# Optimization experiments

Measured on AMD Instinct MI355X. Metric: run time of the kernel, lower is better.

The kernel has to match this reference:

```python
import jax, jax.numpy as jnp
import numpy as np
from jax import lax

B, C, H, W, K = 32, 128, 56, 56, 5
CR = C // 4          # reduced channels in weight-gen MLP
CE = 4 * C           # expanded channels
EPS = 1e-6


def setup_inputs() -> dict:
    key = jax.random.key(0)
    ks = jax.random.split(key, 8)
    s = lambda fan: 1.0 / np.sqrt(fan)
    return {
        "x": jax.random.normal(ks[0], (B, C, H, W), jnp.float32),
        "w_fc1": jax.random.normal(ks[1], (CR, C), jnp.float32) * s(C),
        "ln1_w": jnp.ones((CR,), jnp.float32),
        "ln1_b": jnp.zeros((CR,), jnp.float32),
        "w_fc2": jax.random.normal(ks[2], (C * K * K, CR), jnp.float32) * s(CR),
        "ln2_w": jnp.ones((C,), jnp.float32),
        "ln2_b": jnp.zeros((C,), jnp.float32),
        "w_expand": jax.random.normal(ks[3], (CE, C), jnp.float32) * s(C),
        "w_shrink": jax.random.normal(ks[4], (C, CE), jnp.float32) * s(CE),
        "grn_gamma": jax.random.normal(ks[5], (CE,), jnp.float32) * 0.1,
        "grn_beta": jax.random.normal(ks[6], (CE,), jnp.float32) * 0.1,
    }


def _ln(v, w, b, axis):
    u = v.mean(axis, keepdims=True)
    s2 = jnp.square(v - u).mean(axis, keepdims=True)
    return (v - u) * lax.rsqrt(s2 + EPS) * w + b


def reference(x, w_fc1, ln1_w, ln1_b, w_fc2, ln2_w, ln2_b, w_expand, w_shrink,
              grn_gamma, grn_beta):
    b, c, h, w = x.shape
    # ---- dynamic weight generation: pool -> fc1 -> LN -> fc2 ----
    pooled = x.mean((2, 3))                                  # [B, C]
    hdn = pooled @ w_fc1.T                                   # [B, CR]
    hdn = _ln(hdn, ln1_w, ln1_b, axis=-1)                    # channels_first LN over CR
    dyn = hdn @ w_fc2.T                                      # [B, C*K*K]
    dyn_w = dyn.reshape(b * c, 1, K, K)                      # per-sample depthwise kernels
    # ---- per-sample dynamic depthwise conv (groups = B*C) ----
    pad = K // 2
    out = lax.conv_general_dilated(
        x.reshape(1, b * c, h, w), dyn_w,
        window_strides=(1, 1), padding=[(pad, pad), (pad, pad)],
        dimension_numbers=("NCHW", "OIHW", "NCHW"),
        feature_group_count=b * c,
    ).reshape(b, c, h, w)
    # ---- LN (channels_first) over channel dim ----
    u = out.mean(1, keepdims=True)
    s2 = jnp.square(out - u).mean(1, keepdims=True)
    out = (out - u) * lax.rsqrt(s2 + EPS)
    out = ln2_w[None, :, None, None] * out + ln2_b[None, :, None, None]
    # ---- expand 1x1 -> GELU -> GRN -> shrink 1x1 ----
    out = jnp.einsum("bchw,oc->bohw", out, w_expand)         # [B, 4C, H, W]
    out = jax.nn.gelu(out, approximate=False)
    gx = jnp.sqrt(jnp.sum(jnp.square(out), axis=(2, 3), keepdims=True))  # [B,4C,1,1]
    nx = gx / (gx.mean(1, keepdims=True) + EPS)
    g = grn_gamma[None, :, None, None]
    bt = grn_beta[None, :, None, None]
    out = g * (out * nx) + bt + out
    out = jnp.einsum("bohw,co->bchw", out, w_shrink)         # [B, C, H, W]
    return out + x
```

## Files before the change

### kernel.cpp

```cpp
#include <hip/hip_runtime.h>
#include <hip/hip_bf16.h>

#define B_   32
#define C_   128
#define H_   56
#define W_   56
#define HW_  (H_*W_)
#define BHW_ (B_*HW_)
#define K5_  5
#define KK_  25
#define CR_  32
#define CE_  512
#define EPS_ 1e-6f

typedef __hip_bfloat16 bf16;
typedef __attribute__((ext_vector_type(8))) short short8;
typedef __attribute__((ext_vector_type(4))) float f32x4;


__device__ __forceinline__ float wave_reduce_sum(float v) {
#pragma unroll
  for (int off = 32; off > 0; off >>= 1) v += __shfl_down(v, off, 64);
  return v;
}
__device__ __forceinline__ float bf2f(unsigned short u) {
  return __uint_as_float(((unsigned)u) << 16);
}
__device__ __forceinline__ unsigned short f2bf_bits(float f) {
  bf16 h = __float2bfloat16(f);
  unsigned short u;
  __builtin_memcpy(&u, &h, 2);
  return u;
}
__device__ __forceinline__ float fast_gelu(float v) {
  float t = __expf(-1.702f * v);
  return v * __builtin_amdgcn_rcpf(1.0f + t);
}

__global__ __launch_bounds__(256) void prep_kernel(const float* __restrict__ we,
                                                   bf16* __restrict__ weB) {
  int i = blockIdx.x * 256 + threadIdx.x;
  if (i < CE_ * C_) weB[i] = __float2bfloat16(we[i]);
}

__global__ __launch_bounds__(256) void pool_kernel(const float* __restrict__ x,
                                                   float* __restrict__ pooled) {
  int bc = blockIdx.x;
  const float* xp = x + (size_t)bc * HW_;
  float s = 0.f;
  for (int i = threadIdx.x; i < HW_; i += 256) s += xp[i];
  s = wave_reduce_sum(s);
  __shared__ float red[4];
  int lane = threadIdx.x & 63, wid = threadIdx.x >> 6;
  if (lane == 0) red[wid] = s;
  __syncthreads();
  if (threadIdx.x == 0) pooled[bc] = (red[0] + red[1] + red[2] + red[3]) * (1.0f / HW_);
}

__global__ __launch_bounds__(256) void fc_kernel(const float* __restrict__ pooled,
                                                 const float* __restrict__ w_fc1,
                                                 const float* __restrict__ ln1_w,
                                                 const float* __restrict__ ln1_b,
                                                 const float* __restrict__ w_fc2,
                                                 float* __restrict__ dyn) {
  int b = blockIdx.x;
  int tid = threadIdx.x;
  __shared__ float sp[C_];
  __shared__ float sh[CR_];
  __shared__ float shn[CR_];
  __shared__ float stats[2];
  if (tid < C_) sp[tid] = pooled[b * C_ + tid];
  __syncthreads();
  if (tid < CR_) {
    float acc = 0.f;
    const float* wr = w_fc1 + tid * C_;
#pragma unroll 4
    for (int c = 0; c < C_; ++c) acc += sp[c] * wr[c];
    sh[tid] = acc;
  }
  __syncthreads();
  if (tid == 0) {
    float u = 0.f;
    for (int j = 0; j < CR_; ++j) u += sh[j];
    u *= (1.0f / CR_);
    float v = 0.f;
    for (int j = 0; j < CR_; ++j) { float d = sh[j] - u; v += d * d; }
    v *= (1.0f / CR_);
    stats[0] = u;
    stats[1] = rsqrtf(v + EPS_);
  }
  __syncthreads();
  if (tid < CR_) shn[tid] = (sh[tid] - stats[0]) * stats[1] * ln1_w[tid] + ln1_b[tid];
  __syncthreads();
  for (int i = tid; i < C_ * KK_; i += 256) {
    const float* wr = w_fc2 + i * CR_;
    float acc = 0.f;
#pragma unroll
    for (int j = 0; j < CR_; ++j) acc += shn[j] * wr[j];
    dyn[b * (C_ * KK_) + i] = acc;
  }
}

__global__ __launch_bounds__(256) void conv_kernel(const float* __restrict__ x,
                                                   const float* __restrict__ dyn,
                                                   bf16* __restrict__ z) {
  int bc = blockIdx.x;
  int b = bc >> 7;
  int c = bc & 127;
  int tid = threadIdx.x;
  __shared__ float xs[(H_ + 4) * 64];
  __shared__ float wks[KK_];
  {
    int r = tid >> 6;
    int rr = (r < 2) ? r : (56 + r);
    xs[rr * 64 + (tid & 63)] = 0.f;
  }
  if (tid < 224) {
    int r = tid >> 2, q = tid & 3;
    int col = (q < 2) ? q : (56 + q);
    xs[(r + 2) * 64 + col] = 0.f;
  }
  if (tid < KK_) wks[tid] = dyn[b * (C_ * KK_) + c * KK_ + tid];
  const float4* xp4 = reinterpret_cast<const float4*>(x + (size_t)bc * HW_);
  for (int i = tid; i < 784; i += 256) {
    float4 v = xp4[i];
    int h = i / 14, w4 = (i % 14) * 4;
    float* dst = &xs[(h + 2) * 64 + 2 + w4];
    dst[0] = v.x; dst[1] = v.y; dst[2] = v.z; dst[3] = v.w;
  }
  __syncthreads();
  float wr[KK_];
#pragma unroll
  for (int j = 0; j < KK_; ++j) wr[j] = wks[j];
  for (int g = tid; g < 784; g += 256) {
    int h = g / 14;
    int w4 = (g % 14) * 4;
    float a0 = 0.f, a1 = 0.f, a2 = 0.f, a3 = 0.f;
#pragma unroll
    for (int dh = 0; dh < K5_; ++dh) {
      const float* row = &xs[(h + dh) * 64 + w4];
      float4 va = *reinterpret_cast<const float4*>(row);
      float4 vb = *reinterpret_cast<const float4*>(row + 4);
      float v0 = va.x, v1 = va.y, v2 = va.z, v3 = va.w;
      float v4 = vb.x, v5 = vb.y, v6 = vb.z, v7 = vb.w;
      float u0 = wr[dh * 5 + 0], u1 = wr[dh * 5 + 1], u2 = wr[dh * 5 + 2];
      float u3 = wr[dh * 5 + 3], u4 = wr[dh * 5 + 4];
      a0 += v0 * u0 + v1 * u1 + v2 * u2 + v3 * u3 + v4 * u4;
      a1 += v1 * u0 + v2 * u1 + v3 * u2 + v4 * u3 + v5 * u4;
      a2 += v2 * u0 + v3 * u1 + v4 * u2 + v5 * u3 + v6 * u4;
      a3 += v3 * u0 + v4 * u1 + v5 * u2 + v6 * u3 + v7 * u4;
    }
    size_t base = (size_t)bc * HW_ + h * W_ + w4;
    ushort4 pk = make_ushort4(f2bf_bits(a0), f2bf_bits(a1), f2bf_bits(a2), f2bf_bits(a3));
    *reinterpret_cast<ushort4*>(reinterpret_cast<unsigned short*>(z) + base) = pk;
  }
}

__global__ __launch_bounds__(256) void ln_kernel(const bf16* __restrict__ z,
                                                 const float* __restrict__ ln2_w,
                                                 const float* __restrict__ ln2_b,
                                                 bf16* __restrict__ yT) {
  int hw0 = blockIdx.x * 64;
  int b = blockIdx.y;
  int tid = threadIdx.x;
  int wq = tid & 63;
  int cq = tid >> 6;
  __shared__ unsigned short zt[C_][64];
  __shared__ unsigned short yt[64][136];
  __shared__ float redS[4][64];
  __shared__ float redQ[4][64];
  __shared__ float meanArr[64];
  __shared__ float invArr[64];
  float s = 0.f, q = 0.f;
  const unsigned short* zp = reinterpret_cast<const unsigned short*>(z);
#pragma unroll 4
  for (int k = 0; k < 32; ++k) {
    int c = cq * 32 + k;
    unsigned short u = zp[((size_t)(b * C_ + c)) * HW_ + hw0 + wq];
    float v = bf2f(u);
    s += v;
    q += v * v;
    zt[c][wq] = u;
  }
  redS[cq][wq] = s;
  redQ[cq][wq] = q;
  __syncthreads();
  if (cq == 0) {
    float ss = redS[0][wq] + redS[1][wq] + redS[2][wq] + redS[3][wq];
    float qq = redQ[0][wq] + redQ[1][wq] + redQ[2][wq] + redQ[3][wq];
    float m = ss * (1.0f / C_);
    float var = qq * (1.0f / C_) - m * m;
    meanArr[wq] = m;
    invArr[wq] = rsqrtf(fmaxf(var, 0.f) + EPS_);
  }
  __syncthreads();
  float m = meanArr[wq], iv = invArr[wq];
#pragma unroll
  for (int g = 0; g < 4; ++g) {
    unsigned short pk[8];
#pragma unroll
    for (int i = 0; i < 8; ++i) {
      int c = cq * 32 + g * 8 + i;
      float v = bf2f(zt[c][wq]);
      pk[i] = f2bf_bits((v - m) * iv * ln2_w[c] + ln2_b[c]);
    }
    int4 t;
    __builtin_memcpy(&t, pk, 16);
    *reinterpret_cast<int4*>(&yt[wq][cq * 32 + g * 8]) = t;
  }
  __syncthreads();
  unsigned short* yp = reinterpret_cast<unsigned short*>(yT);
#pragma unroll
  for (int i = 0; i < 4; ++i) {
    int t = tid + 256 * i;
    int row = t >> 4, ch = t & 15;
    int4 v = *reinterpret_cast<const int4*>(&yt[row][ch * 8]);
    *reinterpret_cast<int4*>(yp + ((size_t)(b * HW_ + hw0 + row)) * C_ + ch * 8) = v;
  }
}

__global__ __launch_bounds__(256, 4) void expand_mfma(const bf16* __restrict__ yT,
                                                      const bf16* __restrict__ weB,
                                                      bf16* __restrict__ eT,
                                                      float* __restrict__ gx2) {
  int j0 = blockIdx.x * 128;
  int o0 = blockIdx.y * 128;
  int tid = threadIdx.x;
  int lane = tid & 63, wid = tid >> 6;
  int wm = wid >> 1, wn = wid & 1;
  int quad = lane >> 4, l15 = lane & 15;
  __shared__ __align__(16) char smem[128 * 136 * 2];
  short (*As)[40] = reinterpret_cast<short(*)[40]>(&smem[0]);
  short (*Bs)[40] = reinterpret_cast<short(*)[40]>(&smem[10240]);
  f32x4 acc[4][4] = {};
  const short* yTs = reinterpret_cast<const short*>(yT);
  const short* weS = reinterpret_cast<const short*>(weB);
  for (int k0 = 0; k0 < C_; k0 += 32) {
#pragma unroll
    for (int t = tid; t < 512; t += 256) {
      int r = t >> 2, ch = t & 3;
      int4 va = *reinterpret_cast<const int4*>(yTs + (size_t)(j0 + r) * C_ + k0 + ch * 8);
      *reinterpret_cast<int4*>(&As[r][ch * 8]) = va;
      int4 vb = *reinterpret_cast<const int4*>(weS + (size_t)(o0 + r) * C_ + k0 + ch * 8);
      *reinterpret_cast<int4*>(&Bs[r][ch * 8]) = vb;
    }
    __syncthreads();
    short8 a[4], bfr[4];
#pragma unroll
    for (int mf = 0; mf < 4; ++mf)
      a[mf] = *reinterpret_cast<const short8*>(&As[wm * 64 + mf * 16 + l15][quad * 8]);
#pragma unroll
    for (int nf = 0; nf < 4; ++nf)
      bfr[nf] = *reinterpret_cast<const short8*>(&Bs[wn * 64 + nf * 16 + l15][quad * 8]);
#pragma unroll
    for (int mf = 0; mf < 4; ++mf)
#pragma unroll
      for (int nf = 0; nf < 4; ++nf)
        acc[mf][nf] = __builtin_amdgcn_mfma_f32_16x16x32_bf16(a[mf], bfr[nf], acc[mf][nf], 0, 0, 0);
    __syncthreads();
  }
  short (*Es)[136] = reinterpret_cast<short(*)[136]>(&smem[0]);
#pragma unroll
  for (int mf = 0; mf < 4; ++mf) {
    int jm = j0 + wm * 64 + mf * 16;
    int bb = jm / HW_;
    int jrow = wm * 64 + mf * 16 + quad * 4;
#pragma unroll
    for (int nf = 0; nf < 4; ++nf) {
      int oc = wn * 64 + nf * 16 + l15;
      float g2 = 0.f;
#pragma unroll
      for (int r = 0; r < 4; ++r) {
        float ge = fast_gelu(acc[mf][nf][r]);
        g2 += ge * ge;
        Es[jrow + r][oc] = (short)f2bf_bits(ge);
      }
      g2 += __shfl_xor(g2, 16, 64);
      g2 += __shfl_xor(g2, 32, 64);
      if (quad == 0) atomicAdd(&gx2[bb * CE_ + o0 + oc], g2);
    }
  }
  __syncthreads();
  unsigned short* eP = reinterpret_cast<unsigned short*>(eT);
#pragma unroll
  for (int i = 0; i < 8; ++i) {
    int t = tid + 256 * i;
    int row = t >> 4, ch = t & 15;
    int4 v = *reinterpret_cast<const int4*>(&Es[row][ch * 8]);
    *reinterpret_cast<int4*>(eP + (size_t)(j0 + row) * CE_ + o0 + ch * 8) = v;
  }
}

__global__ __launch_bounds__(512) void grn_scale_kernel(const float* __restrict__ gx2,
                                                        const float* __restrict__ gamma,
                                                        float* __restrict__ scale) {
  int b = blockIdx.x;
  int o = threadIdx.x;
  float gx = sqrtf(gx2[b * CE_ + o]);
  float s = wave_reduce_sum(gx);
  __shared__ float red[8];
  __shared__ float meansh;
  int lane = o & 63, wid = o >> 6;
  if (lane == 0) red[wid] = s;
  __syncthreads();
  if (o == 0) {
    float t = 0.f;
    for (int i = 0; i < 8; ++i) t += red[i];
    meansh = t * (1.0f / CE_);
  }
  __syncthreads();
  scale[b * CE_ + o] = 1.0f + gamma[o] * (gx / (meansh + EPS_));
}

__global__ __launch_bounds__(128) void sb_kernel(const float* __restrict__ w_shrink,
                                                 const float* __restrict__ beta,
                                                 float* __restrict__ sb) {
  int c = threadIdx.x;
  float acc = 0.f;
  for (int o = 0; o < CE_; ++o) acc += w_shrink[c * CE_ + o] * beta[o];
  sb[c] = acc;
}

__global__ __launch_bounds__(256) void scale_ws_kernel(const float* __restrict__ ws,
                                                       const float* __restrict__ scale,
                                                       bf16* __restrict__ sws) {
  int c = blockIdx.x;
  int b = blockIdx.y;
  const float* sp = scale + b * CE_;
  const float* wp = ws + (size_t)c * CE_;
  bf16* op = sws + ((size_t)(b * C_ + c)) * CE_;
  for (int i = threadIdx.x; i < CE_; i += 256)
    op[i] = __float2bfloat16(wp[i] * sp[i]);
}

__global__ __launch_bounds__(256, 4) void shrink_mfma(const bf16* __restrict__ eT,
                                                      const bf16* __restrict__ sws,
                                                      const float* __restrict__ sb,
                                                      const float* __restrict__ x,
                                                      float* __restrict__ out) {
  int hw0 = blockIdx.x * 128;
  int b = blockIdx.y;
  int tid = threadIdx.x;
  int lane = tid & 63, wid = tid >> 6;
  int wm = wid >> 1, wn = wid & 1;
  int quad = lane >> 4, l15 = lane & 15;
  __shared__ __align__(16) char smem[64 * 136 * 4];
  short (*As)[40] = reinterpret_cast<short(*)[40]>(&smem[0]);
  short (*Bs)[40] = reinterpret_cast<short(*)[40]>(&smem[10240]);
  f32x4 acc[4][4] = {};
  const short* eS = reinterpret_cast<const short*>(eT) + (size_t)b * HW_ * CE_;
  const short* wsS = reinterpret_cast<const short*>(sws) + (size_t)b * C_ * CE_;
  for (int k0 = 0; k0 < CE_; k0 += 32) {
#pragma unroll
    for (int t = tid; t < 512; t += 256) {
      int r = t >> 2, ch = t & 3;
      int hwc = hw0 + r; if (hwc >= HW_) hwc = HW_ - 1;
      int4 va = *reinterpret_cast<const int4*>(eS + (size_t)hwc * CE_ + k0 + ch * 8);
      *reinterpret_cast<int4*>(&As[r][ch * 8]) = va;
      int4 vb = *reinterpret_cast<const int4*>(wsS + (size_t)r * CE_ + k0 + ch * 8);
      *reinterpret_cast<int4*>(&Bs[r][ch * 8]) = vb;
    }
    __syncthreads();
    short8 a[4], bfr[4];
#pragma unroll
    for (int mf = 0; mf < 4; ++mf)
      a[mf] = *reinterpret_cast<const short8*>(&As[wm * 64 + mf * 16 + l15][quad * 8]);
#pragma unroll
    for (int nf = 0; nf < 4; ++nf)
      bfr[nf] = *reinterpret_cast<const short8*>(&Bs[wn * 64 + nf * 16 + l15][quad * 8]);
#pragma unroll
    for (int mf = 0; mf < 4; ++mf)
#pragma unroll
      for (int nf = 0; nf < 4; ++nf)
        acc[mf][nf] = __builtin_amdgcn_mfma_f32_16x16x32_bf16(a[mf], bfr[nf], acc[mf][nf], 0, 0, 0);
    __syncthreads();
  }
  float (*Ef)[136] = reinterpret_cast<float(*)[136]>(&smem[0]);
#pragma unroll
  for (int phase = 0; phase < 2; ++phase) {
    if (wn == phase) {
#pragma unroll
      for (int mf = 0; mf < 4; ++mf) {
        int hwr = wm * 64 + mf * 16 + quad * 4;
#pragma unroll
        for (int nf = 0; nf < 4; ++nf) {
          int cr = nf * 16 + l15;
          *reinterpret_cast<f32x4*>(&Ef[cr][hwr]) = acc[mf][nf];
        }
      }
    }
    __syncthreads();
#pragma unroll
    for (int i = 0; i < 8; ++i) {
      int t = tid + 256 * i;
      int row = t >> 5, ch = t & 31;
      int hw = hw0 + ch * 4;
      if (hw < HW_) {
        int c = phase * 64 + row;
        size_t base = ((size_t)(b * C_ + c)) * HW_ + hw;
        float add = sb[c];
        f32x4 av = *reinterpret_cast<const f32x4*>(&Ef[row][ch * 4]);
        float4 xv = *reinterpret_cast<const float4*>(x + base);
        float4 ov;
        ov.x = av.x + add + xv.x;
        ov.y = av.y + add + xv.y;
        ov.z = av.z + add + xv.z;
        ov.w = av.w + add + xv.w;
        *reinterpret_cast<float4*>(out + base) = ov;
      }
    }
    __syncthreads();
  }
}

extern "C" void kernel_launch(void* const* d_in, const int* in_sizes, int n_in,
                              void* d_out, int out_size, void* d_ws, size_t ws_size,
                              hipStream_t stream) {
  (void)in_sizes; (void)n_in; (void)out_size; (void)ws_size;
  const float* x        = (const float*)d_in[0];
  const float* w_fc1    = (const float*)d_in[1];
  const float* ln1_w    = (const float*)d_in[2];
  const float* ln1_b    = (const float*)d_in[3];
  const float* w_fc2    = (const float*)d_in[4];
  const float* ln2_w    = (const float*)d_in[5];
  const float* ln2_b    = (const float*)d_in[6];
  const float* w_expand = (const float*)d_in[7];
  const float* w_shrink = (const float*)d_in[8];
  const float* gamma    = (const float*)d_in[9];
  const float* beta     = (const float*)d_in[10];
  float* out = (float*)d_out;

  char* ws = (char*)d_ws;
  float* pooled = (float*)(ws + 0);
  float* dyn    = (float*)(ws + 16384);
  float* gx2    = (float*)(ws + 425984);
  float* scale  = (float*)(ws + 491520);
  float* sb     = (float*)(ws + 557056);
  bf16*  weB    = (bf16*)(ws + 557568);
  bf16*  yT     = (bf16*)(ws + 819712);
  bf16*  sws    = (bf16*)(ws + 819712);
  bf16*  eT     = (bf16*)(ws + 26509824);
  bf16*  z      = eT;

  prep_kernel<<<256, 256, 0, stream>>>(w_expand, weB);
  pool_kernel<<<B_ * C_, 256, 0, stream>>>(x, pooled);
  fc_kernel<<<B_, 256, 0, stream>>>(pooled, w_fc1, ln1_w, ln1_b, w_fc2, dyn);
  conv_kernel<<<B_ * C_, 256, 0, stream>>>(x, dyn, z);
  ln_kernel<<<dim3(49, B_), 256, 0, stream>>>(z, ln2_w, ln2_b, yT);
  hipMemsetAsync(gx2, 0, B_ * CE_ * sizeof(float), stream);
  expand_mfma<<<dim3(784, 4), 256, 0, stream>>>(yT, weB, eT, gx2);
  grn_scale_kernel<<<B_, 512, 0, stream>>>(gx2, gamma, scale);
  sb_kernel<<<1, 128, 0, stream>>>(w_shrink, beta, sb);
  scale_ws_kernel<<<dim3(C_, B_), 256, 0, stream>>>(w_shrink, scale, sws);
  shrink_mfma<<<dim3(25, B_), 256, 0, stream>>>(eT, sws, sb, x, out);
}
```

Measured before the change: 297.4 us.

## Fuse GRN scaling into shrink GEMM, full-K LDS tiles, merge prep and memset

Removes scale_ws_kernel and instead applies the per-batch GRN scale to the bf16 shrink weights while they are staged into LDS inside shrink_mfma. Both GEMMs now load larger K chunks (the whole 128-wide K for expand, 128-wide chunks for shrink) so there are fewer barriers per tile. Occupancy hints drop to 2 blocks per CU because LDS use grows. The gx2 memset and the w_shrink bf16 conversion are folded into prep_kernel, sb_kernel is parallelised across blocks, and pool_kernel uses float4 loads. This cuts kernel launches and a per-batch weight materialisation, at the cost of lower occupancy and an extra rounding step on the shrink weights (converted to bf16 before scaling).

```diff
diff --git a/kernel.cpp b/kernel.cpp
--- a/kernel.cpp
+++ b/kernel.cpp
@@ -38,17 +38,25 @@
 }
 
 __global__ __launch_bounds__(256) void prep_kernel(const float* __restrict__ we,
-                                                   bf16* __restrict__ weB) {
+                                                   const float* __restrict__ ws,
+                                                   bf16* __restrict__ weB,
+                                                   bf16* __restrict__ wsB,
+                                                   float* __restrict__ gx2) {
   int i = blockIdx.x * 256 + threadIdx.x;
-  if (i < CE_ * C_) weB[i] = __float2bfloat16(we[i]);
+  if (i < CE_ * C_)          weB[i] = __float2bfloat16(we[i]);
+  else if (i < 2 * CE_ * C_) wsB[i - CE_ * C_] = __float2bfloat16(ws[i - CE_ * C_]);
+  else                       gx2[i - 2 * CE_ * C_] = 0.f;
 }
 
 __global__ __launch_bounds__(256) void pool_kernel(const float* __restrict__ x,
                                                    float* __restrict__ pooled) {
   int bc = blockIdx.x;
-  const float* xp = x + (size_t)bc * HW_;
+  const float4* xp4 = reinterpret_cast<const float4*>(x + (size_t)bc * HW_);
   float s = 0.f;
-  for (int i = threadIdx.x; i < HW_; i += 256) s += xp[i];
+  for (int i = threadIdx.x; i < 784; i += 256) {
+    float4 v = xp4[i];
+    s += (v.x + v.y) + (v.z + v.w);
+  }
   s = wave_reduce_sum(s);
   __shared__ float red[4];
   int lane = threadIdx.x & 63, wid = threadIdx.x >> 6;
@@ -219,7 +227,7 @@
   }
 }
 
-__global__ __launch_bounds__(256, 4) void expand_mfma(const bf16* __restrict__ yT,
+__global__ __launch_bounds__(256, 2) void expand_mfma(const bf16* __restrict__ yT,
                                                       const bf16* __restrict__ weB,
                                                       bf16* __restrict__ eT,
                                                       float* __restrict__ gx2) {
@@ -229,37 +237,39 @@
   int lane = tid & 63, wid = tid >> 6;
   int wm = wid >> 1, wn = wid & 1;
   int quad = lane >> 4, l15 = lane & 15;
-  __shared__ __align__(16) char smem[128 * 136 * 2];
-  short (*As)[40] = reinterpret_cast<short(*)[40]>(&smem[0]);
-  short (*Bs)[40] = reinterpret_cast<short(*)[40]>(&smem[10240]);
+  __shared__ __align__(16) char smem[2 * 128 * 136 * 2];
+  short (*As)[136] = reinterpret_cast<short(*)[136]>(smem);
+  short (*Bs)[136] = reinterpret_cast<short(*)[136]>(smem + 34816);
+  const short* yS = reinterpret_cast<const short*>(yT);
+  const short* weS = reinterpret_cast<const short*>(weB);
+#pragma unroll
+  for (int i = 0; i < 8; ++i) {
+    int t = tid + 256 * i;
+    int row = t >> 4, ch = t & 15;
+    *reinterpret_cast<int4*>(&As[row][ch * 8]) =
+        *reinterpret_cast<const int4*>(yS + (size_t)(j0 + row) * C_ + ch * 8);
+    *reinterpret_cast<int4*>(&Bs[row][ch * 8]) =
+        *reinterpret_cast<const int4*>(weS + (size_t)(o0 + row) * C_ + ch * 8);
+  }
+  __syncthreads();
   f32x4 acc[4][4] = {};
-  const short* yTs = reinterpret_cast<const short*>(yT);
-  const short* weS = reinterpret_cast<const short*>(weB);
-  for (int k0 = 0; k0 < C_; k0 += 32) {
-#pragma unroll
-    for (int t = tid; t < 512; t += 256) {
-      int r = t >> 2, ch = t & 3;
-      int4 va = *reinterpret_cast<const int4*>(yTs + (size_t)(j0 + r) * C_ + k0 + ch * 8);
-      *reinterpret_cast<int4*>(&As[r][ch * 8]) = va;
-      int4 vb = *reinterpret_cast<const int4*>(weS + (size_t)(o0 + r) * C_ + k0 + ch * 8);
-      *reinterpret_cast<int4*>(&Bs[r][ch * 8]) = vb;
-    }
-    __syncthreads();
-    short8 a[4], bfr[4];
+#pragma unroll
+  for (int ks = 0; ks < 4; ++ks) {
+    short8 a[4], b[4];
 #pragma unroll
     for (int mf = 0; mf < 4; ++mf)
-      a[mf] = *reinterpret_cast<const short8*>(&As[wm * 64 + mf * 16 + l15][quad * 8]);
+      a[mf] = *reinterpret_cast<const short8*>(&As[wm * 64 + mf * 16 + l15][ks * 32 + quad * 8]);
 #pragma unroll
     for (int nf = 0; nf < 4; ++nf)
-      bfr[nf] = *reinterpret_cast<const short8*>(&Bs[wn * 64 + nf * 16 + l15][quad * 8]);
+      b[nf] = *reinterpret_cast<const short8*>(&Bs[wn * 64 + nf * 16 + l15][ks * 32 + quad * 8]);
 #pragma unroll
     for (int mf = 0; mf < 4; ++mf)
 #pragma unroll
       for (int nf = 0; nf < 4; ++nf)
-        acc[mf][nf] = __builtin_amdgcn_mfma_f32_16x16x32_bf16(a[mf], bfr[nf], acc[mf][nf], 0, 0, 0);
-    __syncthreads();
-  }
-  short (*Es)[136] = reinterpret_cast<short(*)[136]>(&smem[0]);
+        acc[mf][nf] = __builtin_amdgcn_mfma_f32_16x16x32_bf16(a[mf], b[nf], acc[mf][nf], 0, 0, 0);
+  }
+  __syncthreads();
+  short (*Es)[136] = reinterpret_cast<short(*)[136]>(smem);
 #pragma unroll
   for (int mf = 0; mf < 4; ++mf) {
     int jm = j0 + wm * 64 + mf * 16;
@@ -267,17 +277,17 @@
     int jrow = wm * 64 + mf * 16 + quad * 4;
 #pragma unroll
     for (int nf = 0; nf < 4; ++nf) {
-      int oc = wn * 64 + nf * 16 + l15;
+      int ocl = wn * 64 + nf * 16 + l15;
       float g2 = 0.f;
 #pragma unroll
       for (int r = 0; r < 4; ++r) {
         float ge = fast_gelu(acc[mf][nf][r]);
         g2 += ge * ge;
-        Es[jrow + r][oc] = (short)f2bf_bits(ge);
+        Es[jrow + r][ocl] = (short)f2bf_bits(ge);
       }
       g2 += __shfl_xor(g2, 16, 64);
       g2 += __shfl_xor(g2, 32, 64);
-      if (quad == 0) atomicAdd(&gx2[bb * CE_ + o0 + oc], g2);
+      if (quad == 0) atomicAdd(&gx2[bb * CE_ + o0 + ocl], g2);
     }
   }
   __syncthreads();
@@ -312,29 +322,24 @@
   scale[b * CE_ + o] = 1.0f + gamma[o] * (gx / (meansh + EPS_));
 }
 
-__global__ __launch_bounds__(128) void sb_kernel(const float* __restrict__ w_shrink,
+__global__ __launch_bounds__(256) void sb_kernel(const float* __restrict__ w_shrink,
                                                  const float* __restrict__ beta,
                                                  float* __restrict__ sb) {
-  int c = threadIdx.x;
+  int c = blockIdx.x;
+  const float* wp = w_shrink + (size_t)c * CE_;
   float acc = 0.f;
-  for (int o = 0; o < CE_; ++o) acc += w_shrink[c * CE_ + o] * beta[o];
-  sb[c] = acc;
-}
-
-__global__ __launch_bounds__(256) void scale_ws_kernel(const float* __restrict__ ws,
-                                                       const float* __restrict__ scale,
-                                                       bf16* __restrict__ sws) {
-  int c = blockIdx.x;
-  int b = blockIdx.y;
-  const float* sp = scale + b * CE_;
-  const float* wp = ws + (size_t)c * CE_;
-  bf16* op = sws + ((size_t)(b * C_ + c)) * CE_;
-  for (int i = threadIdx.x; i < CE_; i += 256)
-    op[i] = __float2bfloat16(wp[i] * sp[i]);
-}
-
-__global__ __launch_bounds__(256, 4) void shrink_mfma(const bf16* __restrict__ eT,
-                                                      const bf16* __restrict__ sws,
+  for (int o = threadIdx.x; o < CE_; o += 256) acc += wp[o] * beta[o];
+  acc = wave_reduce_sum(acc);
+  __shared__ float red[4];
+  int lane = threadIdx.x & 63, wid = threadIdx.x >> 6;
+  if (lane == 0) red[wid] = acc;
+  __syncthreads();
+  if (threadIdx.x == 0) sb[c] = red[0] + red[1] + red[2] + red[3];
+}
+
+__global__ __launch_bounds__(256, 2) void shrink_mfma(const bf16* __restrict__ eT,
+                                                      const bf16* __restrict__ wsB,
+                                                      const float* __restrict__ scale,
                                                       const float* __restrict__ sb,
                                                       const float* __restrict__ x,
                                                       float* __restrict__ out) {
@@ -344,72 +349,85 @@
   int lane = tid & 63, wid = tid >> 6;
   int wm = wid >> 1, wn = wid & 1;
   int quad = lane >> 4, l15 = lane & 15;
-  __shared__ __align__(16) char smem[64 * 136 * 4];
-  short (*As)[40] = reinterpret_cast<short(*)[40]>(&smem[0]);
-  short (*Bs)[40] = reinterpret_cast<short(*)[40]>(&smem[10240]);
+  __shared__ __align__(16) char smem[2 * 128 * 136 * 2];
+  short (*As)[136] = reinterpret_cast<short(*)[136]>(smem);
+  short (*Bs)[136] = reinterpret_cast<short(*)[136]>(smem + 34816);
+  const short* eS  = reinterpret_cast<const short*>(eT) + (size_t)b * HW_ * CE_;
+  const short* wsS = reinterpret_cast<const short*>(wsB);
+  const float* scp = scale + b * CE_;
   f32x4 acc[4][4] = {};
-  const short* eS = reinterpret_cast<const short*>(eT) + (size_t)b * HW_ * CE_;
-  const short* wsS = reinterpret_cast<const short*>(sws) + (size_t)b * C_ * CE_;
-  for (int k0 = 0; k0 < CE_; k0 += 32) {
-#pragma unroll
-    for (int t = tid; t < 512; t += 256) {
-      int r = t >> 2, ch = t & 3;
-      int hwc = hw0 + r; if (hwc >= HW_) hwc = HW_ - 1;
-      int4 va = *reinterpret_cast<const int4*>(eS + (size_t)hwc * CE_ + k0 + ch * 8);
-      *reinterpret_cast<int4*>(&As[r][ch * 8]) = va;
-      int4 vb = *reinterpret_cast<const int4*>(wsS + (size_t)r * CE_ + k0 + ch * 8);
-      *reinterpret_cast<int4*>(&Bs[r][ch * 8]) = vb;
-    }
-    __syncthreads();
-    short8 a[4], bfr[4];
-#pragma unroll
-    for (int mf = 0; mf < 4; ++mf)
-      a[mf] = *reinterpret_cast<const short8*>(&As[wm * 64 + mf * 16 + l15][quad * 8]);
-#pragma unroll
-    for (int nf = 0; nf < 4; ++nf)
-      bfr[nf] = *reinterpret_cast<const short8*>(&Bs[wn * 64 + nf * 16 + l15][quad * 8]);
-#pragma unroll
-    for (int mf = 0; mf < 4; ++mf)
-#pragma unroll
-      for (int nf = 0; nf < 4; ++nf)
-        acc[mf][nf] = __builtin_amdgcn_mfma_f32_16x16x32_bf16(a[mf], bfr[nf], acc[mf][nf], 0, 0, 0);
-    __syncthreads();
-  }
-  float (*Ef)[136] = reinterpret_cast<float(*)[136]>(&smem[0]);
-#pragma unroll
-  for (int phase = 0; phase < 2; ++phase) {
-    if (wn == phase) {
-#pragma unroll
-      for (int mf = 0; mf < 4; ++mf) {
-        int hwr = wm * 64 + mf * 16 + quad * 4;
-#pragma unroll
-        for (int nf = 0; nf < 4; ++nf) {
-          int cr = nf * 16 + l15;
-          *reinterpret_cast<f32x4*>(&Ef[cr][hwr]) = acc[mf][nf];
-        }
-      }
-    }
-    __syncthreads();
+#pragma unroll 1
+  for (int kc = 0; kc < 4; ++kc) {
+    int k0 = kc * 128;
 #pragma unroll
     for (int i = 0; i < 8; ++i) {
       int t = tid + 256 * i;
-      int row = t >> 5, ch = t & 31;
-      int hw = hw0 + ch * 4;
-      if (hw < HW_) {
-        int c = phase * 64 + row;
-        size_t base = ((size_t)(b * C_ + c)) * HW_ + hw;
-        float add = sb[c];
-        f32x4 av = *reinterpret_cast<const f32x4*>(&Ef[row][ch * 4]);
-        float4 xv = *reinterpret_cast<const float4*>(x + base);
-        float4 ov;
-        ov.x = av.x + add + xv.x;
-        ov.y = av.y + add + xv.y;
-        ov.z = av.z + add + xv.z;
-        ov.w = av.w + add + xv.w;
-        *reinterpret_cast<float4*>(out + base) = ov;
-      }
+      int row = t >> 4, ch = t & 15;
+      int hwc = hw0 + row; if (hwc >= HW_) hwc = HW_ - 1;
+      *reinterpret_cast<int4*>(&As[row][ch * 8]) =
+          *reinterpret_cast<const int4*>(eS + (size_t)hwc * CE_ + k0 + ch * 8);
+      int4 wv = *reinterpret_cast<const int4*>(wsS + (size_t)row * CE_ + k0 + ch * 8);
+      float4 s0 = *reinterpret_cast<const float4*>(scp + k0 + ch * 8);
+      float4 s1 = *reinterpret_cast<const float4*>(scp + k0 + ch * 8 + 4);
+      unsigned short wu[8];
+      __builtin_memcpy(wu, &wv, 16);
+      unsigned short ru[8];
+      ru[0] = f2bf_bits(bf2f(wu[0]) * s0.x);
+      ru[1] = f2bf_bits(bf2f(wu[1]) * s0.y);
+      ru[2] = f2bf_bits(bf2f(wu[2]) * s0.z);
+      ru[3] = f2bf_bits(bf2f(wu[3]) * s0.w);
+      ru[4] = f2bf_bits(bf2f(wu[4]) * s1.x);
+      ru[5] = f2bf_bits(bf2f(wu[5]) * s1.y);
+      ru[6] = f2bf_bits(bf2f(wu[6]) * s1.z);
+      ru[7] = f2bf_bits(bf2f(wu[7]) * s1.w);
+      int4 rv;
+      __builtin_memcpy(&rv, ru, 16);
+      *reinterpret_cast<int4*>(&Bs[row][ch * 8]) = rv;
     }
     __syncthreads();
+#pragma unroll
+    for (int ks = 0; ks < 4; ++ks) {
+      short8 a[4], bfr[4];
+#pragma unroll
+      for (int mf = 0; mf < 4; ++mf)
+        a[mf] = *reinterpret_cast<const short8*>(&As[wm * 64 + mf * 16 + l15][ks * 32 + quad * 8]);
+#pragma unroll
+      for (int nf = 0; nf < 4; ++nf)
+        bfr[nf] = *reinterpret_cast<const short8*>(&Bs[wn * 64 + nf * 16 + l15][ks * 32 + quad * 8]);
+#pragma unroll
+      for (int mf = 0; mf < 4; ++mf)
+#pragma unroll
+        for (int nf = 0; nf < 4; ++nf)
+          acc[mf][nf] = __builtin_amdgcn_mfma_f32_16x16x32_bf16(a[mf], bfr[nf], acc[mf][nf], 0, 0, 0);
+    }
+    __syncthreads();
+  }
+  float (*Ef)[133] = reinterpret_cast<float(*)[133]>(smem);
+#pragma unroll
+  for (int mf = 0; mf < 4; ++mf) {
+    int hwr = wm * 64 + mf * 16 + quad * 4;
+#pragma unroll
+    for (int nf = 0; nf < 4; ++nf)
+      *reinterpret_cast<f32x4*>(&Ef[wn * 64 + nf * 16 + l15][hwr]) = acc[mf][nf];
+  }
+  __syncthreads();
+#pragma unroll
+  for (int i = 0; i < 16; ++i) {
+    int t = tid + 256 * i;
+    int row = t >> 5, ch = t & 31;
+    int hw = hw0 + ch * 4;
+    if (hw < HW_) {
+      size_t base = ((size_t)(b * C_ + row)) * HW_ + hw;
+      float add = sb[row];
+      f32x4 av = *reinterpret_cast<const f32x4*>(&Ef[row][ch * 4]);
+      float4 xv = *reinterpret_cast<const float4*>(x + base);
+      float4 ov;
+      ov.x = av.x + add + xv.x;
+      ov.y = av.y + add + xv.y;
+      ov.z = av.z + add + xv.z;
+      ov.w = av.w + add + xv.w;
+      *reinterpret_cast<float4*>(out + base) = ov;
+    }
   }
 }
 
@@ -437,20 +455,18 @@
   float* scale  = (float*)(ws + 491520);
   float* sb     = (float*)(ws + 557056);
   bf16*  weB    = (bf16*)(ws + 557568);
+  bf16*  wsB    = (bf16*)(ws + 688640);
   bf16*  yT     = (bf16*)(ws + 819712);
-  bf16*  sws    = (bf16*)(ws + 819712);
   bf16*  eT     = (bf16*)(ws + 26509824);
   bf16*  z      = eT;
 
-  prep_kernel<<<256, 256, 0, stream>>>(w_expand, weB);
+  prep_kernel<<<576, 256, 0, stream>>>(w_expand, w_shrink, weB, wsB, gx2);
+  sb_kernel<<<C_, 256, 0, stream>>>(w_shrink, beta, sb);
   pool_kernel<<<B_ * C_, 256, 0, stream>>>(x, pooled);
   fc_kernel<<<B_, 256, 0, stream>>>(pooled, w_fc1, ln1_w, ln1_b, w_fc2, dyn);
   conv_kernel<<<B_ * C_, 256, 0, stream>>>(x, dyn, z);
   ln_kernel<<<dim3(49, B_), 256, 0, stream>>>(z, ln2_w, ln2_b, yT);
-  hipMemsetAsync(gx2, 0, B_ * CE_ * sizeof(float), stream);
   expand_mfma<<<dim3(784, 4), 256, 0, stream>>>(yT, weB, eT, gx2);
   grn_scale_kernel<<<B_, 512, 0, stream>>>(gx2, gamma, scale);
-  sb_kernel<<<1, 128, 0, stream>>>(w_shrink, beta, sb);
-  scale_ws_kernel<<<dim3(C_, B_), 256, 0, stream>>>(w_shrink, scale, sws);
-  shrink_mfma<<<dim3(25, B_), 256, 0, stream>>>(eT, sws, sb, x, out);
-}
+  shrink_mfma<<<dim3(25, B_), 256, 0, stream>>>(eT, wsB, scale, sb, x, out);
+}
```

Result: faster. 273.3 us (-8.1%).
